# Kernel optimization log

Hardware: AMD Instinct MI355X
Metric: run time of the kernel (lower is better)

The kernel has to match this reference:

```python
import jax, jax.numpy as jnp
import numpy as np

NODES, NFEAT = 128, 256


def setup_inputs() -> dict:
    key = jax.random.key(0)
    k1, k2, k3, k4, k5, k6 = jax.random.split(key, 6)
    B = 512
    x = jax.random.normal(k1, (B, NODES, NFEAT), dtype=jnp.float32)
    adj = jax.random.uniform(k2, (B, NODES, NODES), dtype=jnp.float32)
    # GraphConvolution(nfeat, nfeat): weight [nfeat, nfeat], bias [nfeat]
    s = 1.0 / np.sqrt(NFEAT)
    gcn_w = jax.random.uniform(k3, (NFEAT, NFEAT), minval=-s, maxval=s, dtype=jnp.float32)
    gcn_b = jax.random.uniform(k4, (NFEAT,), minval=-s, maxval=s, dtype=jnp.float32)
    # fc: Linear(nfeat*nodes, nfeat), torch layout [out, in]
    s2 = 1.0 / np.sqrt(NFEAT * NODES)
    fc_w = jax.random.uniform(k5, (NFEAT, NFEAT * NODES), minval=-s2, maxval=s2, dtype=jnp.float32)
    fc_b = jax.random.uniform(k6, (NFEAT,), minval=-s2, maxval=s2, dtype=jnp.float32)
    return {"x": x, "adj": adj, "gcn_w": gcn_w, "gcn_b": gcn_b, "fc_w": fc_w, "fc_b": fc_b}


def reference(x, adj, gcn_w, gcn_b, fc_w, fc_b):
    B = x.shape[0]
    # Per-sample loop GCN fused as batched matmuls:
    # support = X @ W ; out = A @ support + b
    support = jnp.einsum('bnf,fg->bng', x, gcn_w)          # [B, nodes, nfeat]
    mid = jnp.einsum('bnm,bmg->bng', adj, support) + gcn_b  # [B, nodes, nfeat]
    # cat along dim0 then reshape(-1, nfeat*nodes) == per-graph flatten
    flat = mid.reshape(B, NODES * NFEAT)
    output = flat @ fc_w.T + fc_b                           # [B, nfeat]
    useful_input = x[:, 0, :]                               # [B, nfeat]
    return (output, useful_input, output)
```

## Files before the change

kernel.cpp:

```cpp
#include <hip/hip_runtime.h>

#define NODES 128
#define NFEAT 256
#define BATCH 512
#define KTOT  (NODES * NFEAT)
#define SPLIT 64
#define KCH   (KTOT / SPLIT)

typedef __bf16 bf16_t;
typedef bf16_t bf16x4 __attribute__((ext_vector_type(4)));
typedef bf16_t bf16x8 __attribute__((ext_vector_type(8)));
typedef float  f32x4  __attribute__((ext_vector_type(4)));

#define BK2   64
#define LDK2  72
#define TILE  128
#define FUSED_BLOCKS 1024
#define CONV_BLOCKS  2048

__device__ __forceinline__ void bar() {
    asm volatile("s_waitcnt lgkmcnt(0)\n\ts_barrier" ::: "memory");
}

__device__ __forceinline__ bf16x8 cvt8(const float4 a, const float4 b) {
    bf16x8 t;
    t[0] = (bf16_t)a.x; t[1] = (bf16_t)a.y; t[2] = (bf16_t)a.z; t[3] = (bf16_t)a.w;
    t[4] = (bf16_t)b.x; t[5] = (bf16_t)b.y; t[6] = (bf16_t)b.z; t[7] = (bf16_t)b.w;
    return t;
}

__device__ __forceinline__ bf16x8 ldcvt(const float* __restrict__ p) {
    const float4 a = *(const float4*)p;
    const float4 b = *(const float4*)(p + 4);
    return cvt8(a, b);
}

struct XT2 { float4 v[8]; };
__device__ __forceinline__ void xload2(const float* __restrict__ src, int ld, int k0,
                                       int tid, XT2& t) {
#pragma unroll
    for (int i = 0; i < 4; i++) {
        int f = tid + i * 256, r = f >> 3, c = f & 7;
        t.v[2 * i]     = *(const float4*)(src + (size_t)r * ld + k0 + c * 8);
        t.v[2 * i + 1] = *(const float4*)(src + (size_t)r * ld + k0 + c * 8 + 4);
    }
}
__device__ __forceinline__ void xstore2(bf16_t* __restrict__ dst, int tid, const XT2& t) {
#pragma unroll
    for (int i = 0; i < 4; i++) {
        int f = tid + i * 256, r = f >> 3, c = f & 7;
        *(bf16x8*)(dst + r * LDK2 + c * 8) = cvt8(t.v[2 * i], t.v[2 * i + 1]);
    }
}

struct AT2 { bf16x8 v[4]; };
__device__ __forceinline__ void aload2(const bf16_t* __restrict__ src, int ld, int k0,
                                       int tid, AT2& t) {
#pragma unroll
    for (int i = 0; i < 4; i++) {
        int f = tid + i * 256, r = f >> 3, c = f & 7;
        t.v[i] = *(const bf16x8*)(src + (size_t)r * ld + k0 + c * 8);
    }
}
__device__ __forceinline__ void astore2(bf16_t* __restrict__ dst, int tid, const AT2& t) {
#pragma unroll
    for (int i = 0; i < 4; i++) {
        int f = tid + i * 256, r = f >> 3, c = f & 7;
        *(bf16x8*)(dst + r * LDK2 + c * 8) = t.v[i];
    }
}

__global__ __launch_bounds__(256)
void k_wt(const float* __restrict__ w, bf16_t* __restrict__ wT) {
    const int g0 = blockIdx.x * 4;
    const int k  = threadIdx.x;
    const float4 v = *(const float4*)(w + (size_t)k * NFEAT + g0);
    wT[(size_t)(g0 + 0) * NFEAT + k] = (bf16_t)v.x;
    wT[(size_t)(g0 + 1) * NFEAT + k] = (bf16_t)v.y;
    wT[(size_t)(g0 + 2) * NFEAT + k] = (bf16_t)v.z;
    wT[(size_t)(g0 + 3) * NFEAT + k] = (bf16_t)v.w;
}

__global__ __launch_bounds__(256, 4)
void k_fused12(const float* __restrict__ x, const float* __restrict__ adj,
               const bf16_t* __restrict__ wT, const float* __restrict__ gcn_b,
               bf16_t* __restrict__ mid,
               const float* __restrict__ fcw, bf16_t* __restrict__ fcwb) {
    __shared__ __align__(16) bf16_t Sb[TILE * 128];

    if (blockIdx.x >= FUSED_BLOCKS) {
        const size_t base = ((size_t)(blockIdx.x - FUSED_BLOCKS) * 256 + threadIdx.x) * 16;
        const float4 a0 = *(const float4*)(fcw + base);
        const float4 a1 = *(const float4*)(fcw + base + 4);
        const float4 a2 = *(const float4*)(fcw + base + 8);
        const float4 a3 = *(const float4*)(fcw + base + 12);
        *(bf16x8*)(fcwb + base)     = cvt8(a0, a1);
        *(bf16x8*)(fcwb + base + 8) = cvt8(a2, a3);
        return;
    }

    const int id  = blockIdx.x;
    const int xcd = id & 7, jj = id >> 3;
    const int b   = (xcd << 6) | (jj >> 1);
    const int n0  = (jj & 1) * TILE;
    const int tid = threadIdx.x;
    const int lane = tid & 63, w = tid >> 6, wm = w & 1, wn = w >> 1;
    const int l15 = lane & 15, q = lane >> 4;
    const float* xb   = x   + (size_t)b * NODES * NFEAT;
    const float* adjb = adj + (size_t)b * NODES * NODES;

    f32x4 acc[4][4] = {};
    {
        const float*  xa = xb + (size_t)(wm * 64 + l15) * NFEAT + q * 8;
        const bf16_t* wp = wT + (size_t)(n0 + wn * 64 + l15) * NFEAT + q * 8;
#pragma unroll
        for (int k = 0; k < 8; k++) {
            bf16x8 bcur[4];
#pragma unroll
            for (int j = 0; j < 4; j++)
                bcur[j] = *(const bf16x8*)(wp + (size_t)j * 16 * NFEAT + k * 32);
#pragma unroll
            for (int i = 0; i < 4; i++) {
                bf16x8 af = ldcvt(xa + (size_t)i * 16 * NFEAT + k * 32);
#pragma unroll
                for (int j = 0; j < 4; j++)
                    acc[i][j] = __builtin_amdgcn_mfma_f32_16x16x32_bf16(af, bcur[j], acc[i][j], 0, 0, 0);
            }
        }
    }

#pragma unroll
    for (int i = 0; i < 4; i++)
#pragma unroll
        for (int j = 0; j < 4; j++) {
            int m = wm * 64 + i * 16 + q * 4;
            int g = wn * 64 + j * 16 + l15;
            int slot = (m >> 3) ^ (g & 15);
            bf16x4 v;
            v[0] = (bf16_t)acc[i][j][0]; v[1] = (bf16_t)acc[i][j][1];
            v[2] = (bf16_t)acc[i][j][2]; v[3] = (bf16_t)acc[i][j][3];
            *(bf16x4*)(&Sb[g * 128 + slot * 8 + (m & 7)]) = v;
        }
    bar();

    f32x4 acc2[4][4] = {};
    {
        const float* aa = adjb + (size_t)(wm * 64 + l15) * NODES + q * 8;
#pragma unroll
        for (int k = 0; k < 4; k++) {
            bf16x8 bb[4];
#pragma unroll
            for (int j = 0; j < 4; j++) {
                int R = wn * 64 + j * 16 + l15;
                int slot = (k * 4 + q) ^ (R & 15);
                bb[j] = *(const bf16x8*)(&Sb[R * 128 + slot * 8]);
            }
#pragma unroll
            for (int i = 0; i < 4; i++) {
                bf16x8 af = ldcvt(aa + (size_t)i * 16 * NODES + k * 32);
#pragma unroll
                for (int j = 0; j < 4; j++)
                    acc2[i][j] = __builtin_amdgcn_mfma_f32_16x16x32_bf16(af, bb[j], acc2[i][j], 0, 0, 0);
            }
        }
    }

    bf16_t* outb = mid + (size_t)b * NODES * NFEAT;
#pragma unroll
    for (int j = 0; j < 4; j++) {
        int g = n0 + wn * 64 + j * 16 + l15;
        float bias = gcn_b[g];
#pragma unroll
        for (int i = 0; i < 4; i++)
#pragma unroll
            for (int rr = 0; rr < 4; rr++) {
                int node = wm * 64 + i * 16 + q * 4 + rr;
                outb[(size_t)node * NFEAT + g] = (bf16_t)(acc2[i][j][rr] + bias);
            }
    }
}

__global__ __launch_bounds__(256, 2)
void k_out_bf(const bf16_t* __restrict__ flat, const bf16_t* __restrict__ fcwb,
              bf16_t* __restrict__ part) {
    __shared__ __align__(16) bf16_t As[2][TILE * LDK2];
    __shared__ __align__(16) bf16_t Bs[2][TILE * LDK2];
    const int m0 = blockIdx.x * TILE;
    const int n0 = blockIdx.y * TILE;
    const int kb = blockIdx.z * KCH;
    const int tid = threadIdx.x;
    const int lane = tid & 63, w = tid >> 6, wm = w & 1, wn = w >> 1;
    const int l15 = lane & 15, q = lane >> 4;
    f32x4 acc[4][4] = {};
    const bf16_t* fa = flat + (size_t)m0 * KTOT;
    const bf16_t* fb = fcwb + (size_t)n0 * KTOT;

    AT2 ra[3], rb[2];
    aload2(fa, KTOT, kb + 0 * BK2, tid, ra[0]);
    aload2(fb, KTOT, kb + 0 * BK2, tid, rb[0]);
    aload2(fa, KTOT, kb + 1 * BK2, tid, ra[1]);
    aload2(fb, KTOT, kb + 1 * BK2, tid, rb[1]);
    aload2(fa, KTOT, kb + 2 * BK2, tid, ra[2]);
    astore2(As[0], tid, ra[0]);
    astore2(Bs[0], tid, rb[0]);
    bar();
#pragma unroll
    for (int k = 0; k < 8; k++) {
        if (k + 3 < 8) aload2(fa, KTOT, kb + (k + 3) * BK2, tid, ra[k % 3]);
        if (k + 2 < 8) aload2(fb, KTOT, kb + (k + 2) * BK2, tid, rb[k & 1]);
#pragma unroll
        for (int kk = 0; kk < BK2; kk += 32) {
            bf16x8 a[4], bbf[4];
#pragma unroll
            for (int i = 0; i < 4; i++)
                a[i] = *(const bf16x8*)(&As[k & 1][(wm * 64 + i * 16 + l15) * LDK2 + kk + q * 8]);
#pragma unroll
            for (int j = 0; j < 4; j++)
                bbf[j] = *(const bf16x8*)(&Bs[k & 1][(wn * 64 + j * 16 + l15) * LDK2 + kk + q * 8]);
#pragma unroll
            for (int i = 0; i < 4; i++)
#pragma unroll
                for (int j = 0; j < 4; j++)
                    acc[i][j] = __builtin_amdgcn_mfma_f32_16x16x32_bf16(a[i], bbf[j], acc[i][j], 0, 0, 0);
        }
        if (k + 1 < 8) {
            astore2(As[(k + 1) & 1], tid, ra[(k + 1) % 3]);
            astore2(Bs[(k + 1) & 1], tid, rb[(k + 1) & 1]);
        }
        bar();
    }
    bf16_t* pb = part + (size_t)blockIdx.z * BATCH * NFEAT;
#pragma unroll
    for (int i = 0; i < 4; i++)
#pragma unroll
        for (int j = 0; j < 4; j++)
#pragma unroll
            for (int r = 0; r < 4; r++) {
                int bt_ = m0 + wm * 64 + i * 16 + q * 4 + r;
                int o   = n0 + wn * 64 + j * 16 + l15;
                pb[(size_t)bt_ * NFEAT + o] = (bf16_t)acc[i][j][r];
            }
}

__global__ __launch_bounds__(256, 2)
void k_out(const bf16_t* __restrict__ flat, const float* __restrict__ fcw,
           bf16_t* __restrict__ part) {
    __shared__ __align__(16) bf16_t As[2][TILE * LDK2];
    __shared__ __align__(16) bf16_t Bs[2][TILE * LDK2];
    const int m0 = blockIdx.x * TILE;
    const int n0 = blockIdx.y * TILE;
    const int kb = blockIdx.z * KCH;
    const int tid = threadIdx.x;
    const int lane = tid & 63, w = tid >> 6, wm = w & 1, wn = w >> 1;
    const int l15 = lane & 15, q = lane >> 4;
    f32x4 acc[4][4] = {};
    const bf16_t* fa = flat + (size_t)m0 * KTOT;
    const float*  fb = fcw + (size_t)n0 * KTOT;

    AT2 ra[3]; XT2 rb[2];
    aload2(fa, KTOT, kb + 0 * BK2, tid, ra[0]);
    xload2(fb, KTOT, kb + 0 * BK2, tid, rb[0]);
    aload2(fa, KTOT, kb + 1 * BK2, tid, ra[1]);
    xload2(fb, KTOT, kb + 1 * BK2, tid, rb[1]);
    aload2(fa, KTOT, kb + 2 * BK2, tid, ra[2]);
    astore2(As[0], tid, ra[0]);
    xstore2(Bs[0], tid, rb[0]);
    bar();
#pragma unroll
    for (int k = 0; k < 8; k++) {
        if (k + 3 < 8) aload2(fa, KTOT, kb + (k + 3) * BK2, tid, ra[k % 3]);
        if (k + 2 < 8) xload2(fb, KTOT, kb + (k + 2) * BK2, tid, rb[k & 1]);
#pragma unroll
        for (int kk = 0; kk < BK2; kk += 32) {
            bf16x8 a[4], bbf[4];
#pragma unroll
            for (int i = 0; i < 4; i++)
                a[i] = *(const bf16x8*)(&As[k & 1][(wm * 64 + i * 16 + l15) * LDK2 + kk + q * 8]);
#pragma unroll
            for (int j = 0; j < 4; j++)
                bbf[j] = *(const bf16x8*)(&Bs[k & 1][(wn * 64 + j * 16 + l15) * LDK2 + kk + q * 8]);
#pragma unroll
            for (int i = 0; i < 4; i++)
#pragma unroll
                for (int j = 0; j < 4; j++)
                    acc[i][j] = __builtin_amdgcn_mfma_f32_16x16x32_bf16(a[i], bbf[j], acc[i][j], 0, 0, 0);
        }
        if (k + 1 < 8) {
            astore2(As[(k + 1) & 1], tid, ra[(k + 1) % 3]);
            xstore2(Bs[(k + 1) & 1], tid, rb[(k + 1) & 1]);
        }
        bar();
    }
    bf16_t* pb = part + (size_t)blockIdx.z * BATCH * NFEAT;
#pragma unroll
    for (int i = 0; i < 4; i++)
#pragma unroll
        for (int j = 0; j < 4; j++)
#pragma unroll
            for (int r = 0; r < 4; r++) {
                int bt_ = m0 + wm * 64 + i * 16 + q * 4 + r;
                int o   = n0 + wn * 64 + j * 16 + l15;
                pb[(size_t)bt_ * NFEAT + o] = (bf16_t)acc[i][j][r];
            }
}

__global__ __launch_bounds__(256)
void k_reduce(const bf16_t* __restrict__ part, const float* __restrict__ fc_b,
              const float* __restrict__ x, float* __restrict__ out) {
    const int g4 = (blockIdx.x * 256 + threadIdx.x) * 4;
    const int o = g4 & (NFEAT - 1), b = g4 >> 8;
    float s[4];
    const float4 c0 = *(const float4*)(fc_b + o);
    s[0] = c0.x; s[1] = c0.y; s[2] = c0.z; s[3] = c0.w;
#pragma unroll 8
    for (int i = 0; i < SPLIT; i++) {
        bf16x4 p = *(const bf16x4*)(part + (size_t)i * BATCH * NFEAT + g4);
#pragma unroll
        for (int j = 0; j < 4; j++) s[j] += (float)p[j];
    }
    float4 o0 = make_float4(s[0], s[1], s[2], s[3]);
    *(float4*)(out + g4) = o0;
    *(float4*)(out + 2 * BATCH * NFEAT + g4) = o0;
    *(float4*)(out + BATCH * NFEAT + g4) = *(const float4*)(x + (size_t)b * NODES * NFEAT + o);
}

extern "C" void kernel_launch(void* const* d_in, const int* in_sizes, int n_in,
                              void* d_out, int out_size, void* d_ws, size_t ws_size,
                              hipStream_t stream) {
    const float* x     = (const float*)d_in[0];
    const float* adj   = (const float*)d_in[1];
    const float* gcn_w = (const float*)d_in[2];
    const float* gcn_b = (const float*)d_in[3];
    const float* fc_w  = (const float*)d_in[4];
    const float* fc_b  = (const float*)d_in[5];
    float* out = (float*)d_out;

    const size_t midB  = (size_t)BATCH * NODES * NFEAT * 2;
    const size_t partB = (size_t)SPLIT * BATCH * NFEAT * 2;
    const size_t fcwB  = (size_t)NFEAT * KTOT * 2;
    bf16_t* wT   = (bf16_t*)d_ws;
    bf16_t* mid  = (bf16_t*)((char*)d_ws + 131072);
    bf16_t* part = (bf16_t*)((char*)d_ws + 131072 + midB);
    bf16_t* fcwb = (bf16_t*)((char*)d_ws + 131072 + midB + partB);
    const bool cv = ws_size >= 131072 + midB + partB + fcwB;

    k_wt     <<<dim3(64), dim3(256), 0, stream>>>(gcn_w, wT);
    k_fused12<<<dim3(cv ? FUSED_BLOCKS + CONV_BLOCKS : FUSED_BLOCKS), dim3(256), 0, stream>>>(
        x, adj, wT, gcn_b, mid, fc_w, fcwb);
    if (cv)
        k_out_bf<<<dim3(4, 2, SPLIT), dim3(256), 0, stream>>>(mid, fcwb, part);
    else
        k_out   <<<dim3(4, 2, SPLIT), dim3(256), 0, stream>>>(mid, fc_w, part);
    k_reduce <<<dim3(128), dim3(256), 0, stream>>>(part, fc_b, x, out);
}
```

Measured before the change: 228.9 us.

## Stage x and adj tiles through double-buffered LDS with register prefetch in fused GCN kernel

Both GEMM phases of the fused GCN kernel now stage fp32 x and adj tiles cooperatively into a double-buffered bf16 LDS buffer. Register prefetch runs three K-steps ahead, replacing per-wave direct global loads with conversion in the inner loop. This should cut redundant global traffic, since each wave pair no longer reloads the same A rows, and it overlaps loads with MFMA. It also drops the XCD-aware block-to-batch remap and lowers the occupancy hint from 4 to 3 blocks per CU. The cost is extra LDS, more registers for the prefetch buffers, and one barrier per K-step.

```diff
diff --git a/kernel.cpp b/kernel.cpp
--- a/kernel.cpp
+++ b/kernel.cpp
@@ -12,6 +12,8 @@
 typedef bf16_t bf16x8 __attribute__((ext_vector_type(8)));
 typedef float  f32x4  __attribute__((ext_vector_type(4)));
 
+#define BK    32
+#define LDK   40
 #define BK2   64
 #define LDK2  72
 #define TILE  128
@@ -29,10 +31,22 @@
     return t;
 }
 
-__device__ __forceinline__ bf16x8 ldcvt(const float* __restrict__ p) {
-    const float4 a = *(const float4*)p;
-    const float4 b = *(const float4*)(p + 4);
-    return cvt8(a, b);
+struct XT { float4 v[4]; };
+__device__ __forceinline__ void xload(const float* __restrict__ src, int ld, int k0,
+                                      int tid, XT& t) {
+#pragma unroll
+    for (int i = 0; i < 2; i++) {
+        int f = tid + i * 256, r = f >> 2, c = f & 3;
+        t.v[2 * i]     = *(const float4*)(src + (size_t)r * ld + k0 + c * 8);
+        t.v[2 * i + 1] = *(const float4*)(src + (size_t)r * ld + k0 + c * 8 + 4);
+    }
+}
+__device__ __forceinline__ void xstore(bf16_t* __restrict__ dst, int tid, const XT& t) {
+#pragma unroll
+    for (int i = 0; i < 2; i++) {
+        int f = tid + i * 256, r = f >> 2, c = f & 3;
+        *(bf16x8*)(dst + r * LDK + c * 8) = cvt8(t.v[2 * i], t.v[2 * i + 1]);
+    }
 }
 
 struct XT2 { float4 v[8]; };
@@ -81,12 +95,13 @@
     wT[(size_t)(g0 + 3) * NFEAT + k] = (bf16_t)v.w;
 }
 
-__global__ __launch_bounds__(256, 4)
+__global__ __launch_bounds__(256, 3)
 void k_fused12(const float* __restrict__ x, const float* __restrict__ adj,
                const bf16_t* __restrict__ wT, const float* __restrict__ gcn_b,
                bf16_t* __restrict__ mid,
                const float* __restrict__ fcw, bf16_t* __restrict__ fcwb) {
-    __shared__ __align__(16) bf16_t Sb[TILE * 128];
+    __shared__ __align__(16) bf16_t As[2][TILE * LDK];
+    __shared__ __align__(16) bf16_t Sb[TILE * TILE];
 
     if (blockIdx.x >= FUSED_BLOCKS) {
         const size_t base = ((size_t)(blockIdx.x - FUSED_BLOCKS) * 256 + threadIdx.x) * 16;
@@ -99,36 +114,51 @@
         return;
     }
 
-    const int id  = blockIdx.x;
-    const int xcd = id & 7, jj = id >> 3;
-    const int b   = (xcd << 6) | (jj >> 1);
-    const int n0  = (jj & 1) * TILE;
+    const int n0  = (blockIdx.x & 1) * TILE;
+    const int b   = blockIdx.x >> 1;
     const int tid = threadIdx.x;
     const int lane = tid & 63, w = tid >> 6, wm = w & 1, wn = w >> 1;
     const int l15 = lane & 15, q = lane >> 4;
     const float* xb   = x   + (size_t)b * NODES * NFEAT;
     const float* adjb = adj + (size_t)b * NODES * NODES;
 
+    const bf16_t* wrow[4];
+#pragma unroll
+    for (int j = 0; j < 4; j++)
+        wrow[j] = wT + (size_t)(n0 + wn * 64 + j * 16 + l15) * NFEAT + q * 8;
+
     f32x4 acc[4][4] = {};
     {
-        const float*  xa = xb + (size_t)(wm * 64 + l15) * NFEAT + q * 8;
-        const bf16_t* wp = wT + (size_t)(n0 + wn * 64 + l15) * NFEAT + q * 8;
+        XT r[3];
+        xload(xb, NFEAT, 0 * BK, tid, r[0]);
+        xload(xb, NFEAT, 1 * BK, tid, r[1]);
+        xload(xb, NFEAT, 2 * BK, tid, r[2]);
+        xstore(As[0], tid, r[0]);
+        bar();
 #pragma unroll
         for (int k = 0; k < 8; k++) {
+            if (k + 3 < 8) xload(xb, NFEAT, (k + 3) * BK, tid, r[k % 3]);
             bf16x8 bcur[4];
 #pragma unroll
-            for (int j = 0; j < 4; j++)
-                bcur[j] = *(const bf16x8*)(wp + (size_t)j * 16 * NFEAT + k * 32);
-#pragma unroll
-            for (int i = 0; i < 4; i++) {
-                bf16x8 af = ldcvt(xa + (size_t)i * 16 * NFEAT + k * 32);
+            for (int j = 0; j < 4; j++) bcur[j] = *(const bf16x8*)(wrow[j] + k * BK);
+            bf16x8 a[4];
+#pragma unroll
+            for (int i = 0; i < 4; i++)
+                a[i] = *(const bf16x8*)(&As[k & 1][(wm * 64 + i * 16 + l15) * LDK + q * 8]);
+#pragma unroll
+            for (int i = 0; i < 4; i++)
 #pragma unroll
                 for (int j = 0; j < 4; j++)
-                    acc[i][j] = __builtin_amdgcn_mfma_f32_16x16x32_bf16(af, bcur[j], acc[i][j], 0, 0, 0);
-            }
-        }
-    }
-
+                    acc[i][j] = __builtin_amdgcn_mfma_f32_16x16x32_bf16(a[i], bcur[j], acc[i][j], 0, 0, 0);
+            if (k + 1 < 8) xstore(As[(k + 1) & 1], tid, r[(k + 1) % 3]);
+            bar();
+        }
+    }
+
+    XT r[3];
+    xload(adjb, NODES, 0 * BK, tid, r[0]);
+    xload(adjb, NODES, 1 * BK, tid, r[1]);
+    xload(adjb, NODES, 2 * BK, tid, r[2]);
 #pragma unroll
     for (int i = 0; i < 4; i++)
 #pragma unroll
@@ -142,29 +172,31 @@
             *(bf16x4*)(&Sb[g * 128 + slot * 8 + (m & 7)]) = v;
         }
     bar();
+    xstore(As[0], tid, r[0]);
+    bar();
 
     f32x4 acc2[4][4] = {};
-    {
-        const float* aa = adjb + (size_t)(wm * 64 + l15) * NODES + q * 8;
-#pragma unroll
-        for (int k = 0; k < 4; k++) {
-            bf16x8 bb[4];
-#pragma unroll
-            for (int j = 0; j < 4; j++) {
-                int R = wn * 64 + j * 16 + l15;
-                int slot = (k * 4 + q) ^ (R & 15);
-                bb[j] = *(const bf16x8*)(&Sb[R * 128 + slot * 8]);
-            }
-#pragma unroll
-            for (int i = 0; i < 4; i++) {
-                bf16x8 af = ldcvt(aa + (size_t)i * 16 * NODES + k * 32);
-#pragma unroll
-                for (int j = 0; j < 4; j++)
-                    acc2[i][j] = __builtin_amdgcn_mfma_f32_16x16x32_bf16(af, bb[j], acc2[i][j], 0, 0, 0);
-            }
-        }
-    }
-
+#pragma unroll
+    for (int k = 0; k < 4; k++) {
+        if (k + 3 < 4) xload(adjb, NODES, (k + 3) * BK, tid, r[k % 3]);
+        bf16x8 a[4], bb[4];
+#pragma unroll
+        for (int i = 0; i < 4; i++)
+            a[i] = *(const bf16x8*)(&As[k & 1][(wm * 64 + i * 16 + l15) * LDK + q * 8]);
+#pragma unroll
+        for (int j = 0; j < 4; j++) {
+            int R = wn * 64 + j * 16 + l15;
+            int slot = (k * 4 + q) ^ (R & 15);
+            bb[j] = *(const bf16x8*)(&Sb[R * 128 + slot * 8]);
+        }
+#pragma unroll
+        for (int i = 0; i < 4; i++)
+#pragma unroll
+            for (int j = 0; j < 4; j++)
+                acc2[i][j] = __builtin_amdgcn_mfma_f32_16x16x32_bf16(a[i], bb[j], acc2[i][j], 0, 0, 0);
+        if (k + 1 < 4) xstore(As[(k + 1) & 1], tid, r[(k + 1) % 3]);
+        bar();
+    }
     bf16_t* outb = mid + (size_t)b * NODES * NFEAT;
 #pragma unroll
     for (int j = 0; j < 4; j++) {
```

After: 195.8 us. 14.5% less time.
